# Optimization experiments

Hardware: AMD Instinct MI355X
Metric: run time of the kernel (lower is better)

## Reference

```python
import jax, jax.numpy as jnp
import numpy as np

NUM_USERS = 100000
NUM_ITEMS = 50000
DIM = 64
HOP = 3
NNZ = 4_000_000
BATCH = 4096
NUM_NEG = 8
N = NUM_USERS + NUM_ITEMS


def setup_inputs() -> dict:
    key = jax.random.key(0)
    ks = jax.random.split(key, 8)
    user_emb = jax.random.normal(ks[0], (NUM_USERS, DIM), dtype=jnp.float32) * 0.1
    item_emb = jax.random.normal(ks[1], (NUM_ITEMS, DIM), dtype=jnp.float32) * 0.1
    # normalized-Laplacian-like small positive values
    A_vals = jax.random.uniform(ks[2], (NNZ,), dtype=jnp.float32) * 0.02
    A_rows = jax.random.randint(ks[3], (NNZ,), 0, N, dtype=jnp.int32)
    A_cols = jax.random.randint(ks[4], (NNZ,), 0, N, dtype=jnp.int32)
    users = jax.random.randint(ks[5], (BATCH,), 0, NUM_USERS, dtype=jnp.int32)
    items = jax.random.randint(ks[6], (BATCH,), 0, NUM_ITEMS, dtype=jnp.int32)
    negatives = jax.random.randint(ks[7], (NUM_NEG * BATCH,), 0, NUM_ITEMS, dtype=jnp.int32)
    return {"user_emb": user_emb, "item_emb": item_emb, "A_vals": A_vals,
            "A_rows": A_rows, "A_cols": A_cols,
            "users": users, "items": items, "negatives": negatives}


def _computer(user_emb, item_emb, A_vals, A_rows, A_cols):
    # LightGCN propagation: x_{k+1} = A @ x_k, mean over hops 0..HOP
    all_emb = jnp.concatenate([user_emb, item_emb], axis=0)  # [N, D]
    x = all_emb
    acc = all_emb
    for _ in range(HOP):
        # SpMM: gather source rows, scale by edge value, scatter-add to dest
        msgs = A_vals[:, None] * x[A_cols]                      # [nnz, D]
        x = jax.ops.segment_sum(msgs, A_rows, num_segments=N)   # [N, D]
        acc = acc + x
    light_out = acc / jnp.asarray(HOP + 1, dtype=all_emb.dtype)
    return light_out[:NUM_USERS], light_out[NUM_USERS:]


def reference(user_emb, item_emb, A_vals, A_rows, A_cols, users, items, negatives):
    all_users_emb, all_items_emb = _computer(user_emb, item_emb, A_vals, A_rows, A_cols)
    users_emb = all_users_emb[users]          # [B, D]
    items_emb = all_items_emb[items]          # [B, D]
    neg_item_embs = all_items_emb[negatives]  # [NUM_NEG*B, D]
    pos_scores = jnp.sum(users_emb * items_emb, axis=1)  # [B]
    pos_exp = jnp.exp(pos_scores)
    neg_k = jnp.sum(users_emb[None, :, :] * neg_item_embs.reshape(NUM_NEG, BATCH, DIM), axis=-1)  # [NUM_NEG, B]
    neg_exp = jnp.sum(jnp.exp(neg_k), axis=0)  # [B]
    info_nce = jnp.mean(-jnp.log(pos_exp / (pos_exp + neg_exp)))
    return info_nce
```

## Files before the change

kernel.cpp:

```cpp
#include <hip/hip_runtime.h>
#include <hip/hip_bf16.h>
#include <hip/hip_fp8.h>


#define NUM_USERS 100000
#define NUM_ITEMS 50000
#define NTOT      150000
#define DIM       64
#define NNZ_C     4000000
#define BATCH     4096
#define NUM_NEG   8
#define NSLICE    (BATCH + BATCH + NUM_NEG * BATCH)

#define RPB        384
#define NBUCKET    ((NTOT + RPB - 1) / RPB)
#define CAP        11264
#define CAPC       11776
#define BIN_BLOCKS 1024
#define EPB        ((NNZ_C + BIN_BLOCKS - 1) / BIN_BLOCKS)

using fp8t = __hip_fp8_e4m3;

typedef unsigned int u32x4 __attribute__((ext_vector_type(4)));
typedef float        f32x2 __attribute__((ext_vector_type(2)));

__device__ __forceinline__ float f8dec(unsigned char b) {
    fp8t h; h.__x = (__hip_fp8_storage_t)b; return (float)h;
}
__device__ __forceinline__ unsigned char f8enc(float f) {
    fp8t h(f); return (unsigned char)h.__x;
}

__device__ __forceinline__ void fp8x4_fma(unsigned int q, float w, float* a) {
#if __has_builtin(__builtin_amdgcn_cvt_pk_f32_fp8)
    f32x2 lo = __builtin_amdgcn_cvt_pk_f32_fp8((int)q, false);
    f32x2 hi = __builtin_amdgcn_cvt_pk_f32_fp8((int)q, true);
    a[0] = fmaf(w, lo.x, a[0]);
    a[1] = fmaf(w, lo.y, a[1]);
    a[2] = fmaf(w, hi.x, a[2]);
    a[3] = fmaf(w, hi.y, a[3]);
#else
    a[0] = fmaf(w, f8dec((unsigned char)(q       & 0xFF)), a[0]);
    a[1] = fmaf(w, f8dec((unsigned char)((q>>8)  & 0xFF)), a[1]);
    a[2] = fmaf(w, f8dec((unsigned char)((q>>16) & 0xFF)), a[2]);
    a[3] = fmaf(w, f8dec((unsigned char)((q>>24) & 0xFF)), a[3]);
#endif
}

__global__ void convert_concat(const float* __restrict__ ue, const float* __restrict__ ie,
                               unsigned char* __restrict__ x0, float* __restrict__ loss_accum,
                               int* __restrict__ bcur) {
    int i = blockIdx.x * blockDim.x + threadIdx.x;
    if (i == 0) loss_accum[0] = 0.0f;
    if (i < NBUCKET) bcur[i * 16] = i * CAP;
    if (i >= NTOT * DIM / 4) return;
    float4 v = (i * 4 < NUM_USERS * DIM)
                   ? ((const float4*)ue)[i]
                   : ((const float4*)ie)[i - NUM_USERS * DIM / 4];
    uchar4 o;
    o.x = f8enc(v.x); o.y = f8enc(v.y); o.z = f8enc(v.z); o.w = f8enc(v.w);
    ((uchar4*)x0)[i] = o;
}

__global__ void __launch_bounds__(256) bin_k(const int* __restrict__ rows,
                                             const int* __restrict__ cols,
                                             const float* __restrict__ vals,
                                             int* __restrict__ bcur,
                                             int2* __restrict__ brec) {
    __shared__ int2 stage[EPB];
    __shared__ int  pdst[EPB];
    __shared__ int  lh[NBUCKET], gbase[NBUCKET];
    __shared__ unsigned short lofs[NBUCKET];
    int t = threadIdx.x;
    int* sm = (int*)stage;
    int e0 = blockIdx.x * EPB;
    int e1 = e0 + EPB; if (e1 > NNZ_C) e1 = NNZ_C;
    for (int i = t; i < NBUCKET; i += 256) lh[i] = 0;
    __syncthreads();
    #pragma unroll 4
    for (int e = e0 + t; e < e1; e += 256)
        atomicAdd(&lh[__builtin_nontemporal_load(rows + e) / RPB], 1);
    __syncthreads();
    {
        int loc[2];
        int ssum = 0;
        #pragma unroll
        for (int k = 0; k < 2; ++k) {
            int i = t * 2 + k;
            loc[k] = (i < NBUCKET) ? lh[i] : 0;
            ssum += loc[k];
        }
        sm[t] = ssum;
        __syncthreads();
        for (int o = 1; o < 256; o <<= 1) {
            int v = (t >= o) ? sm[t - o] : 0;
            __syncthreads();
            sm[t] += v;
            __syncthreads();
        }
        int run = sm[t] - ssum;
        #pragma unroll
        for (int k = 0; k < 2; ++k) {
            int i = t * 2 + k;
            if (i < NBUCKET) lofs[i] = (unsigned short)run;
            run += loc[k];
        }
    }
    __syncthreads();
    for (int i = t; i < NBUCKET; i += 256) {
        int c = lh[i];
        gbase[i] = c ? atomicAdd(&bcur[i * 16], c) : 0;
        lh[i] = 0;
    }
    __syncthreads();
    #pragma unroll 2
    for (int e = e0 + t; e < e1; e += 256) {
        int   r = __builtin_nontemporal_load(rows + e);
        int   c = __builtin_nontemporal_load(cols + e);
        float v = __builtin_nontemporal_load(vals + e);
        int b = r / RPB;
        int rank = atomicAdd(&lh[b], 1);
        int j = (int)lofs[b] + rank;
        stage[j] = make_int2(((r - b * RPB) << 18) | c, __float_as_int(v));
        pdst[j]  = gbase[b] + rank;
    }
    __syncthreads();
    int cnt = e1 - e0;
    for (int j = t; j < cnt; j += 256)
        brec[pdst[j]] = stage[j];
}

__global__ void csr_fix_k(const int2* __restrict__ brec, const int* __restrict__ bcur,
                          unsigned int* __restrict__ crec, int2* __restrict__ rp2) {
    __shared__ int lh[RPB], lb[RPB], lc[RPB], sm2[256];
    int b = blockIdx.x;
    int t = threadIdx.x;
    int s = b * CAP, e = bcur[b * 16];
    int cnt = e - s;
    int cb = b * CAPC;
    for (int i = t; i < RPB; i += 256) lh[i] = 0;
    __syncthreads();
    for (int j = t; j < cnt; j += 256)
        atomicAdd(&lh[(brec[s + j].x >> 18) & 511], 1);
    __syncthreads();
    {
        int loc[2];
        int ssum = 0;
        #pragma unroll
        for (int k = 0; k < 2; ++k) {
            int i = t * 2 + k;
            loc[k] = (i < RPB) ? ((lh[i] + 3) & ~3) : 0;
            ssum += loc[k];
        }
        sm2[t] = ssum;
        __syncthreads();
        for (int o = 1; o < 256; o <<= 1) {
            int v = (t >= o) ? sm2[t - o] : 0;
            __syncthreads();
            sm2[t] += v;
            __syncthreads();
        }
        int run = sm2[t] - ssum;
        #pragma unroll
        for (int k = 0; k < 2; ++k) {
            int i = t * 2 + k;
            if (i < RPB) {
                lb[i] = run;
                lc[i] = 0;
                int row = b * RPB + i;
                if (row < NTOT) rp2[row] = make_int2(cb + run, cb + run + lh[i]);
            }
            run += loc[k];
        }
    }
    __syncthreads();
    for (int j = t; j < cnt; j += 256) {
        int2 rc = brec[s + j];
        int rl = (rc.x >> 18) & 511;
        int pos = atomicAdd(&lc[rl], 1);
        float v = __int_as_float(rc.y);
        unsigned int v14 = (unsigned int)lrintf(v * 524288.0f);
        if (v14 > 16383u) v14 = 16383u;
        crec[cb + lb[rl] + pos] = (v14 << 18) | (unsigned int)(rc.x & 0x3FFFF);
    }
    __syncthreads();
    for (int i = t; i < RPB; i += 256) {
        int base = cb + lb[i];
        int c4 = (lh[i] + 3) & ~3;
        for (int q = lh[i]; q < c4; ++q) crec[base + q] = 0u;
    }
}

__device__ __forceinline__ void spmm_row_v3(const unsigned char* __restrict__ x,
                                            const unsigned int* __restrict__ crec,
                                            int s, int e, int lane, float* acc) {
    const float c19 = 1.9073486328125e-6f;
    int g  = lane >> 4;
    int dq = (lane & 15) * 4;
    acc[0] = acc[1] = acc[2] = acc[3] = 0.0f;
    int e4 = s + ((e - s + 3) & ~3);
    for (int j = s + 4 * g; j < e4; j += 16) {
        u32x4 p = __builtin_nontemporal_load((const u32x4*)(crec + j));
        unsigned int q0 = *(const unsigned int*)(x + (p.x & 0x3FFFFu) * DIM + dq);
        unsigned int q1 = *(const unsigned int*)(x + (p.y & 0x3FFFFu) * DIM + dq);
        unsigned int q2 = *(const unsigned int*)(x + (p.z & 0x3FFFFu) * DIM + dq);
        unsigned int q3 = *(const unsigned int*)(x + (p.w & 0x3FFFFu) * DIM + dq);
        float w0 = (float)(p.x >> 18) * c19;
        float w1 = (float)(p.y >> 18) * c19;
        float w2 = (float)(p.z >> 18) * c19;
        float w3 = (float)(p.w >> 18) * c19;
        fp8x4_fma(q0, w0, acc);
        fp8x4_fma(q1, w1, acc);
        fp8x4_fma(q2, w2, acc);
        fp8x4_fma(q3, w3, acc);
    }
    acc[0] += __shfl_xor(acc[0], 16, 64);
    acc[1] += __shfl_xor(acc[1], 16, 64);
    acc[2] += __shfl_xor(acc[2], 16, 64);
    acc[3] += __shfl_xor(acc[3], 16, 64);
    acc[0] += __shfl_xor(acc[0], 32, 64);
    acc[1] += __shfl_xor(acc[1], 32, 64);
    acc[2] += __shfl_xor(acc[2], 32, 64);
    acc[3] += __shfl_xor(acc[3], 32, 64);
}

__device__ __forceinline__ void spmm_store(unsigned char* __restrict__ y, int row,
                                           int lane, const float* acc) {
    if (lane < 16) {
        uchar4 o;
        o.x = f8enc(acc[0] * 16.0f);
        o.y = f8enc(acc[1] * 16.0f);
        o.z = f8enc(acc[2] * 16.0f);
        o.w = f8enc(acc[3] * 16.0f);
        *(uchar4*)(y + row * DIM + lane * 4) = o;
    }
}

__global__ void spmm_k(const unsigned char* __restrict__ x, const int2* __restrict__ rp2,
                       const unsigned int* __restrict__ crec, unsigned char* __restrict__ y) {
    int row  = (blockIdx.x * blockDim.x + threadIdx.x) >> 6;
    int lane = threadIdx.x & 63;
    if (row >= NTOT) return;
    int2 se = rp2[row];
    float acc[4];
    spmm_row_v3(x, crec, se.x, se.y, lane, acc);
    spmm_store(y, row, lane, acc);
}

__global__ void spmm_sliced_k(const unsigned char* __restrict__ x, const int2* __restrict__ rp2,
                              const unsigned int* __restrict__ crec,
                              const int* __restrict__ users, const int* __restrict__ items,
                              const int* __restrict__ negs, unsigned char* __restrict__ y) {
    int w    = (blockIdx.x * blockDim.x + threadIdx.x) >> 6;
    int lane = threadIdx.x & 63;
    if (w >= NSLICE) return;
    int row = (w < BATCH)     ? users[w]
            : (w < 2 * BATCH) ? NUM_USERS + items[w - BATCH]
                              : NUM_USERS + negs[w - 2 * BATCH];
    int2 se = rp2[row];
    float acc[4];
    spmm_row_v3(x, crec, se.x, se.y, lane, acc);
    spmm_store(y, row, lane, acc);
}

__global__ void loss_k(const unsigned char* __restrict__ x0, const unsigned char* __restrict__ x1,
                       const unsigned char* __restrict__ x2, const unsigned char* __restrict__ x3,
                       const int* __restrict__ users, const int* __restrict__ items,
                       const int* __restrict__ negs, float* __restrict__ loss_accum) {
    int w    = (blockIdx.x * blockDim.x + threadIdx.x) >> 6;
    int lane = threadIdx.x & 63;
    if (w >= BATCH) return;
    auto rowv = [&](int r) -> float {
        int o = r * DIM + lane;
        return 0.25f * f8dec(x0[o]) + 0.015625f * f8dec(x1[o]) +
               9.765625e-4f * f8dec(x2[o]) + 6.103515625e-5f * f8dec(x3[o]);
    };
    float ue = rowv(users[w]);
    float ie = rowv(NUM_USERS + items[w]);
    float p = ue * ie;
    for (int o = 32; o > 0; o >>= 1) p += __shfl_xor(p, o, 64);
    float pe = expf(p);
    float ne = 0.0f;
    for (int k = 0; k < NUM_NEG; ++k) {
        float q = ue * rowv(NUM_USERS + negs[k * BATCH + w]);
        for (int o = 32; o > 0; o >>= 1) q += __shfl_xor(q, o, 64);
        ne += expf(q);
    }
    if (lane == 0) atomicAdd(loss_accum, logf((pe + ne) / pe));
}

__global__ void finalize_k(const float* __restrict__ loss_accum, float* __restrict__ out) {
    out[0] = loss_accum[0] * (1.0f / BATCH);
}

__global__ void sentinel_k(float* __restrict__ out) {
    out[0] = -1.0f;
}

extern "C" void kernel_launch(void* const* d_in, const int* in_sizes, int n_in,
                              void* d_out, int out_size, void* d_ws, size_t ws_size,
                              hipStream_t stream) {
    const float* user_emb = (const float*)d_in[0];
    const float* item_emb = (const float*)d_in[1];
    const float* A_vals   = (const float*)d_in[2];
    const int*   A_rows   = (const int*)d_in[3];
    const int*   A_cols   = (const int*)d_in[4];
    const int*   users    = (const int*)d_in[5];
    const int*   items    = (const int*)d_in[6];
    const int*   negs     = (const int*)d_in[7];
    float* out = (float*)d_out;

    char* ws = (char*)d_ws;
    size_t off = 0;
    auto carve = [&](size_t bytes) -> char* {
        char* p = ws + off;
        off = (off + bytes + 255) & ~(size_t)255;
        return p;
    };
    unsigned char* x0 = (unsigned char*)carve((size_t)NTOT * DIM);
    unsigned char* x1 = (unsigned char*)carve((size_t)NTOT * DIM);
    unsigned char* x2 = (unsigned char*)carve((size_t)NTOT * DIM);
    unsigned char* x3 = (unsigned char*)carve((size_t)NTOT * DIM);
    int2*  brec       = (int2*)carve((size_t)NBUCKET * CAP * 8);
    unsigned int* crec= (unsigned int*)carve((size_t)NBUCKET * CAPC * 4 + 1024);
    int2*  rp2        = (int2*)carve((size_t)NTOT * 8);
    int*   bcur       = (int*)carve((size_t)NBUCKET * 64);
    float* loss_accum = (float*)carve(256);

    if (off > ws_size) {
        sentinel_k<<<1, 1, 0, stream>>>(out);
        return;
    }

    convert_concat<<<(NTOT * DIM / 4 + 255) / 256, 256, 0, stream>>>(user_emb, item_emb, x0, loss_accum, bcur);

    bin_k<<<BIN_BLOCKS, 256, 0, stream>>>(A_rows, A_cols, A_vals, bcur, brec);
    csr_fix_k<<<NBUCKET, 256, 0, stream>>>(brec, bcur, crec, rp2);

    const int spmm_blocks = (NTOT * 64 + 255) / 256;
    spmm_k<<<spmm_blocks, 256, 0, stream>>>(x0, rp2, crec, x1);
    spmm_k<<<spmm_blocks, 256, 0, stream>>>(x1, rp2, crec, x2);
    spmm_sliced_k<<<(NSLICE * 64 + 255) / 256, 256, 0, stream>>>(x2, rp2, crec, users, items, negs, x3);

    loss_k<<<(BATCH * 64 + 255) / 256, 256, 0, stream>>>(x0, x1, x2, x3, users, items, negs, loss_accum);
    finalize_k<<<1, 1, 0, stream>>>(loss_accum, out);
}
```

Measured before the change: 448.3 us.

## Widen CSR buckets, pad bin chunks, move value quantization into binning

Doubles rows per bucket to 768, which halves the bucket count so each binning block needs a single-element scan per thread. Chunks claimed from each global bucket are padded to multiples of 8 with sentinel records, which aligns the scattered writes. The per-edge destination array in shared memory is dropped, and the destination is recomputed from the stored row instead. Value quantization to 14 bits moves from the CSR fix pass into the binning pass, and the fix kernel runs with 512 threads, skipping padding records by range-checking the row. The costs are extra padding writes and larger per-bucket capacity buffers.

```diff
diff --git a/kernel.cpp b/kernel.cpp
--- a/kernel.cpp
+++ b/kernel.cpp
@@ -12,10 +12,10 @@
 #define NUM_NEG   8
 #define NSLICE    (BATCH + BATCH + NUM_NEG * BATCH)
 
-#define RPB        384
+#define RPB        768
 #define NBUCKET    ((NTOT + RPB - 1) / RPB)
-#define CAP        11264
-#define CAPC       11776
+#define CAP        25600
+#define CAPC       23296
 #define BIN_BLOCKS 1024
 #define EPB        ((NNZ_C + BIN_BLOCKS - 1) / BIN_BLOCKS)
 
@@ -68,7 +68,6 @@
                                              int* __restrict__ bcur,
                                              int2* __restrict__ brec) {
     __shared__ int2 stage[EPB];
-    __shared__ int  pdst[EPB];
     __shared__ int  lh[NBUCKET], gbase[NBUCKET];
     __shared__ unsigned short lofs[NBUCKET];
     int t = threadIdx.x;
@@ -82,14 +81,7 @@
         atomicAdd(&lh[__builtin_nontemporal_load(rows + e) / RPB], 1);
     __syncthreads();
     {
-        int loc[2];
-        int ssum = 0;
-        #pragma unroll
-        for (int k = 0; k < 2; ++k) {
-            int i = t * 2 + k;
-            loc[k] = (i < NBUCKET) ? lh[i] : 0;
-            ssum += loc[k];
-        }
+        int ssum = (t < NBUCKET) ? lh[t] : 0;
         sm[t] = ssum;
         __syncthreads();
         for (int o = 1; o < 256; o <<= 1) {
@@ -98,18 +90,18 @@
             sm[t] += v;
             __syncthreads();
         }
-        int run = sm[t] - ssum;
-        #pragma unroll
-        for (int k = 0; k < 2; ++k) {
-            int i = t * 2 + k;
-            if (i < NBUCKET) lofs[i] = (unsigned short)run;
-            run += loc[k];
-        }
+        if (t < NBUCKET) lofs[t] = (unsigned short)(sm[t] - ssum);
     }
     __syncthreads();
     for (int i = t; i < NBUCKET; i += 256) {
         int c = lh[i];
-        gbase[i] = c ? atomicAdd(&bcur[i * 16], c) : 0;
+        if (c) {
+            int c8 = (c + 7) & ~7;
+            int g  = atomicAdd(&bcur[i * 16], c8);
+            gbase[i] = g;
+            for (int q = g + c; q < g + c8; ++q)
+                brec[q] = make_int2(0, -1);
+        }
         lh[i] = 0;
     }
     __syncthreads();
@@ -121,27 +113,36 @@
         int b = r / RPB;
         int rank = atomicAdd(&lh[b], 1);
         int j = (int)lofs[b] + rank;
-        stage[j] = make_int2(((r - b * RPB) << 18) | c, __float_as_int(v));
-        pdst[j]  = gbase[b] + rank;
+        unsigned int v14 = (unsigned int)lrintf(v * 524288.0f);
+        if (v14 > 16383u) v14 = 16383u;
+        stage[j] = make_int2((int)((v14 << 18) | (unsigned int)c), r);
     }
     __syncthreads();
     int cnt = e1 - e0;
-    for (int j = t; j < cnt; j += 256)
-        brec[pdst[j]] = stage[j];
-}
-
-__global__ void csr_fix_k(const int2* __restrict__ brec, const int* __restrict__ bcur,
-                          unsigned int* __restrict__ crec, int2* __restrict__ rp2) {
-    __shared__ int lh[RPB], lb[RPB], lc[RPB], sm2[256];
+    for (int j = t; j < cnt; j += 256) {
+        int2 rc = stage[j];
+        int b = rc.y / RPB;
+        brec[gbase[b] + (j - (int)lofs[b])] = rc;
+    }
+}
+
+__global__ void __launch_bounds__(512) csr_fix_k(const int2* __restrict__ brec,
+                                                 const int* __restrict__ bcur,
+                                                 unsigned int* __restrict__ crec,
+                                                 int2* __restrict__ rp2) {
+    __shared__ int lh[RPB], lb[RPB], lc[RPB], sm2[512];
     int b = blockIdx.x;
     int t = threadIdx.x;
     int s = b * CAP, e = bcur[b * 16];
     int cnt = e - s;
     int cb = b * CAPC;
-    for (int i = t; i < RPB; i += 256) lh[i] = 0;
-    __syncthreads();
-    for (int j = t; j < cnt; j += 256)
-        atomicAdd(&lh[(brec[s + j].x >> 18) & 511], 1);
+    int rbase = b * RPB;
+    for (int i = t; i < RPB; i += 512) lh[i] = 0;
+    __syncthreads();
+    for (int j = t; j < cnt; j += 512) {
+        unsigned int rl = (unsigned int)(brec[s + j].y - rbase);
+        if (rl < RPB) atomicAdd(&lh[rl], 1);
+    }
     __syncthreads();
     {
         int loc[2];
@@ -154,7 +155,7 @@
         }
         sm2[t] = ssum;
         __syncthreads();
-        for (int o = 1; o < 256; o <<= 1) {
+        for (int o = 1; o < 512; o <<= 1) {
             int v = (t >= o) ? sm2[t - o] : 0;
             __syncthreads();
             sm2[t] += v;
@@ -167,24 +168,23 @@
             if (i < RPB) {
                 lb[i] = run;
                 lc[i] = 0;
-                int row = b * RPB + i;
+                int row = rbase + i;
                 if (row < NTOT) rp2[row] = make_int2(cb + run, cb + run + lh[i]);
             }
             run += loc[k];
         }
     }
     __syncthreads();
-    for (int j = t; j < cnt; j += 256) {
+    for (int j = t; j < cnt; j += 512) {
         int2 rc = brec[s + j];
-        int rl = (rc.x >> 18) & 511;
-        int pos = atomicAdd(&lc[rl], 1);
-        float v = __int_as_float(rc.y);
-        unsigned int v14 = (unsigned int)lrintf(v * 524288.0f);
-        if (v14 > 16383u) v14 = 16383u;
-        crec[cb + lb[rl] + pos] = (v14 << 18) | (unsigned int)(rc.x & 0x3FFFF);
-    }
-    __syncthreads();
-    for (int i = t; i < RPB; i += 256) {
+        unsigned int rl = (unsigned int)(rc.y - rbase);
+        if (rl < RPB) {
+            int pos = atomicAdd(&lc[rl], 1);
+            crec[cb + lb[rl] + pos] = (unsigned int)rc.x;
+        }
+    }
+    __syncthreads();
+    for (int i = t; i < RPB; i += 512) {
         int base = cb + lb[i];
         int c4 = (lh[i] + 3) & ~3;
         for (int q = lh[i]; q < c4; ++q) crec[base + q] = 0u;
@@ -335,7 +335,7 @@
     convert_concat<<<(NTOT * DIM / 4 + 255) / 256, 256, 0, stream>>>(user_emb, item_emb, x0, loss_accum, bcur);
 
     bin_k<<<BIN_BLOCKS, 256, 0, stream>>>(A_rows, A_cols, A_vals, bcur, brec);
-    csr_fix_k<<<NBUCKET, 256, 0, stream>>>(brec, bcur, crec, rp2);
+    csr_fix_k<<<NBUCKET, 512, 0, stream>>>(brec, bcur, crec, rp2);
 
     const int spmm_blocks = (NTOT * 64 + 255) / 256;
     spmm_k<<<spmm_blocks, 256, 0, stream>>>(x0, rp2, crec, x1);
```

Measured after the change: 438.9 us. 1.02x faster.
